# Performance work log

Measured on AMD Instinct MI355X. Metric: run time of the kernel, lower is better.

## Reference

```python
import jax, jax.numpy as jnp
import numpy as np

B, N, D, DG = 32, 2048, 512, 1024


def layernorm(x, g, b, eps=1e-5):
    m = jnp.mean(x, axis=-1, keepdims=True)
    v = jnp.mean((x - m) ** 2, axis=-1, keepdims=True)
    return (x - m) * jax.lax.rsqrt(v + eps) * g + b


def simple_rms_norm(x, eps=1e-6):
    # parameter-free RMSNorm used inside Hgru1d
    return x * jax.lax.rsqrt(jnp.mean(x * x, axis=-1, keepdims=True) + eps)


def linear_recurrence(lam, u, reverse):
    # h_t = lam_t * h_{t-1} + u_t along axis=1, via associative scan
    def comb(c1, c2):
        a1, b1 = c1
        a2, b2 = c2
        return a1 * a2, a2 * b1 + b2
    return jax.lax.associative_scan(comb, (lam, u), axis=1, reverse=reverse)[1]


def hgru1d(x, lower_bound, Wi, bi, Wf, bf, Wg, bg, Wo, bo):
    # HGRN-style gated recurrence, bidirectional (causal=False, shared params)
    i = jax.nn.silu(x @ Wi + bi)                       # candidate input  [b,n,d]
    f = jax.nn.sigmoid(x @ Wf + bf)                    # forget gate      [b,n,d]
    lam = lower_bound + (1.0 - lower_bound) * f        # lower-bounded decay
    u = (1.0 - lam) * i
    h = linear_recurrence(lam, u, False) + linear_recurrence(lam, u, True)
    h = simple_rms_norm(h)
    g = jax.nn.sigmoid(x @ Wg + bg)                    # output gate
    return (h * g) @ Wo + bo


def glu(x, W1, b1, W2, b2, W3, b3):
    return (jax.nn.silu(x @ W1 + b1) * (x @ W2 + b2)) @ W3 + b3


def setup_inputs() -> dict:
    key = jax.random.key(0)
    ks = jax.random.split(key, 16)
    s = 0.02
    return {
        "x": jax.random.normal(ks[0], (B, N, D), dtype=jnp.float32),
        "lower_bound": 0,
        "Wi": jax.random.normal(ks[1], (D, D), jnp.float32) * s,
        "bi": jnp.zeros((D,), jnp.float32),
        "Wf": jax.random.normal(ks[2], (D, D), jnp.float32) * s,
        "bf": jnp.zeros((D,), jnp.float32),
        "Wg": jax.random.normal(ks[3], (D, D), jnp.float32) * s,
        "bg": jnp.zeros((D,), jnp.float32),
        "Wo": jax.random.normal(ks[4], (D, D), jnp.float32) * s,
        "bo": jnp.zeros((D,), jnp.float32),
        "tn_g": jnp.ones((D,), jnp.float32),
        "tn_b": jnp.zeros((D,), jnp.float32),
        "fn_g": jnp.ones((D,), jnp.float32),
        "fn_b": jnp.zeros((D,), jnp.float32),
        "W1": jax.random.normal(ks[5], (D, DG), jnp.float32) * s,
        "b1": jnp.zeros((DG,), jnp.float32),
        "W2": jax.random.normal(ks[6], (D, DG), jnp.float32) * s,
        "b2": jnp.zeros((DG,), jnp.float32),
        "W3": jax.random.normal(ks[7], (DG, D), jnp.float32) * s,
        "b3": jnp.zeros((D,), jnp.float32),
    }


def reference(x, lower_bound, Wi, bi, Wf, bf, Wg, bg, Wo, bo,
              tn_g, tn_b, fn_g, fn_b, W1, b1, W2, b2, W3, b3):
    lb = jnp.float32(lower_bound)
    # post-norm residual block
    x = x + layernorm(hgru1d(x, lb, Wi, bi, Wf, bf, Wg, bg, Wo, bo), tn_g, tn_b)
    x = x + layernorm(glu(x, W1, b1, W2, b2, W3, b3), fn_g, fn_b)
    return x
```

## Files before the change

kernel.cpp:

```cpp
#include <hip/hip_runtime.h>
#include <hip/hip_bf16.h>

#define BB 32
#define NN 2048
#define DD 512
#define DGG 1024
#define CC 32
#define LLEN 64

typedef short bf16x8 __attribute__((ext_vector_type(8)));
typedef float f32x4  __attribute__((ext_vector_type(4)));

__device__ __forceinline__ unsigned short f2bf(float f){
    __hip_bfloat16 h = __float2bfloat16(f);
    return *reinterpret_cast<unsigned short*>(&h);
}
__device__ __forceinline__ float bf2f(unsigned short u){
    unsigned int x = ((unsigned int)u) << 16;
    return __uint_as_float(x);
}
__device__ __forceinline__ float sigm(float x){ return 1.0f/(1.0f + __expf(-x)); }

__device__ __forceinline__ void gl_lds16(const unsigned short* g, unsigned short* l){
    __builtin_amdgcn_global_load_lds(
        (const __attribute__((address_space(1))) unsigned int*)g,
        (__attribute__((address_space(3))) unsigned int*)l, 16, 0, 0);
}

__global__ __launch_bounds__(256)
void wt_prep(const float* __restrict__ in, unsigned short* __restrict__ out,
             int K, int N)
{
    __shared__ float t[32][33];
    const int tid = threadIdx.x;
    const int r = tid >> 3;
    const int c = (tid & 7) << 2;
    const int n0 = blockIdx.x * 32;
    const int k0 = blockIdx.y * 32;
    float4 v = *(const float4*)(in + (size_t)(k0 + r) * N + n0 + c);
    t[r][c] = v.x; t[r][c+1] = v.y; t[r][c+2] = v.z; t[r][c+3] = v.w;
    __syncthreads();
    ushort4 o;
    o.x = f2bf(t[c+0][r]); o.y = f2bf(t[c+1][r]);
    o.z = f2bf(t[c+2][r]); o.w = f2bf(t[c+3][r]);
    *(ushort4*)(out + (size_t)(n0 + r) * K + k0 + c) = o;
}

__global__ __launch_bounds__(256)
void wt_prep_pair(const float* __restrict__ in0, const float* __restrict__ in1,
                  unsigned short* __restrict__ out, int K, int N)
{
    __shared__ float t[32][33];
    const int tid = threadIdx.x;
    const int bx  = blockIdx.x;
    const int k0  = blockIdx.y * 32;
    const int kk  = tid >> 3;
    const int rq  = (tid & 7) << 2;
    const float* src = ((rq >> 4) & 1) ? in1 : in0;
    const int c0 = bx * 16 + (rq & 15);
    float4 v = *(const float4*)(src + (size_t)(k0 + kk) * N + c0);
    t[kk][rq] = v.x; t[kk][rq+1] = v.y; t[kk][rq+2] = v.z; t[kk][rq+3] = v.w;
    __syncthreads();
    const int rr = tid >> 3;
    const int kc = (tid & 7) << 2;
    ushort4 o;
    o.x = f2bf(t[kc+0][rr]); o.y = f2bf(t[kc+1][rr]);
    o.z = f2bf(t[kc+2][rr]); o.w = f2bf(t[kc+3][rr]);
    *(ushort4*)(out + (size_t)(bx * 32 + rr) * K + k0 + kc) = o;
}

__global__ __launch_bounds__(256)
void cast_bf16(const float* __restrict__ in, unsigned short* __restrict__ out)
{
    size_t i = ((size_t)blockIdx.x * 256 + threadIdx.x) * 4;
    float4 v = *(const float4*)(in + i);
    ushort4 o;
    o.x = f2bf(v.x); o.y = f2bf(v.y); o.z = f2bf(v.z); o.w = f2bf(v.w);
    *(ushort4*)(out + i) = o;
}

template<int MODE, int K, int NI>
__global__ __launch_bounds__(512, 2)
void gemm256(const unsigned short* __restrict__ A,
             const unsigned short* __restrict__ Bt,
             const float* __restrict__ bias0,
             const float* __restrict__ bias1,
             unsigned short* __restrict__ out0,
             unsigned short* __restrict__ out1,
             const int* __restrict__ lbp, int Mtiles)
{
    constexpr int NT   = K / 32;
    constexpr int Ntl  = NI / 256;
    constexpr int NOUT = (MODE >= 5) ? NI / 2 : NI;
    constexpr int TILE = 256 * 32;
    __shared__ unsigned short As0[TILE], As1[TILE], As2[TILE], As3[TILE];
    __shared__ unsigned short Bs0[TILE], Bs1[TILE], Bs2[TILE], Bs3[TILE];
#define ASL(i) ((i)==0?As0:(i)==1?As1:(i)==2?As2:As3)
#define BSL(i) ((i)==0?Bs0:(i)==1?Bs1:(i)==2?Bs2:Bs3)

    const int tid  = threadIdx.x;
    const int wave = tid >> 6;
    const int lane = tid & 63;
    const int lm   = lane & 15;
    const int quad = lane >> 4;
    const int wr   = (wave >> 2) * 128;
    const int wc   = (wave & 3) * 64;

    const int nwg = Mtiles * Ntl;
    const int h   = blockIdx.x;
    const int wg  = (h & 7) * (nwg >> 3) + (h >> 3);
    const int bm  = wg / Ntl;
    const int bn  = wg - bm * Ntl;
    const size_t m0 = (size_t)bm * 256;
    const int    n0 = bn * 256;

    const int lrow  = lane >> 2;
    const int oslot = ((lane & 3) ^ ((lane >> 3) & 3)) << 3;
    const unsigned short* gA = A  + (m0 + (size_t)(wave * 16 + lrow)) * K + oslot;
    const unsigned short* gB = Bt + ((size_t)n0 + wave * 16 + lrow) * K + oslot;
    const int lbase = (wave * 16) * 32;
    const int aslot = (quad ^ ((lm >> 1) & 3)) << 3;

#define STAGE(kt, i) do {                                               \
        const unsigned short* ga_ = gA + (kt) * 32;                     \
        const unsigned short* gb_ = gB + (kt) * 32;                     \
        gl_lds16(ga_,                  ASL(i) + lbase);                 \
        gl_lds16(ga_ + (size_t)128*K,  ASL(i) + lbase + 128*32);        \
        gl_lds16(gb_,                  BSL(i) + lbase);                 \
        gl_lds16(gb_ + (size_t)128*K,  BSL(i) + lbase + 128*32);        \
    } while (0)

    f32x4 acc[8][4];
    const f32x4 zero = {0.f, 0.f, 0.f, 0.f};
    #pragma unroll
    for (int i = 0; i < 8; ++i)
        #pragma unroll
        for (int j = 0; j < 4; ++j) acc[i][j] = zero;

    STAGE(0, 0);
    STAGE(1, 1);
    STAGE(2, 2);
    asm volatile("s_waitcnt vmcnt(8)" ::: "memory");
    __builtin_amdgcn_s_barrier();

    #pragma unroll
    for (int t = 0; t < NT; ++t) {
        if (t + 3 < NT) STAGE(t + 3, (t + 3) & 3);

        const unsigned short* Ab = ASL(t & 3);
        const unsigned short* Bb = BSL(t & 3);
        bf16x8 a[8], b[4];
        #pragma unroll
        for (int mi = 0; mi < 8; ++mi)
            a[mi] = *(const bf16x8*)&Ab[(wr + mi * 16 + lm) * 32 + aslot];
        #pragma unroll
        for (int ni = 0; ni < 4; ++ni)
            b[ni] = *(const bf16x8*)&Bb[(wc + ni * 16 + lm) * 32 + aslot];
        #pragma unroll
        for (int mi = 0; mi < 8; ++mi)
            #pragma unroll
            for (int ni = 0; ni < 4; ++ni)
                acc[mi][ni] = __builtin_amdgcn_mfma_f32_16x16x32_bf16(
                    a[mi], b[ni], acc[mi][ni], 0, 0, 0);

        if (t + 1 < NT) {
            if (t + 3 < NT)      asm volatile("s_waitcnt vmcnt(8)" ::: "memory");
            else if (t + 2 < NT) asm volatile("s_waitcnt vmcnt(4)" ::: "memory");
            else                 asm volatile("s_waitcnt vmcnt(0)" ::: "memory");
            __builtin_amdgcn_s_barrier();
        }
    }
#undef STAGE
#undef ASL
#undef BSL

    float lbv = 0.f;
    if constexpr (MODE == 5) lbv = (float)(*lbp);

    if constexpr (MODE == 5 || MODE == 6) {
        const int cbase = (n0 + wc) >> 1;
        #pragma unroll
        for (int nip = 0; nip < 4; nip += 2) {
            const int c = cbase + (nip >> 1) * 16 + lm;
            const float b0 = bias0[c];
            const float b1v = bias1[c];
            #pragma unroll
            for (int mi = 0; mi < 8; ++mi) {
                #pragma unroll
                for (int r = 0; r < 4; ++r) {
                    const size_t row = m0 + wr + mi * 16 + quad * 4 + r;
                    const size_t oidx = row * NOUT + c;
                    float p0 = acc[mi][nip][r]     + b0;
                    float p1 = acc[mi][nip + 1][r] + b1v;
                    if constexpr (MODE == 5) {
                        float si = p0 * sigm(p0);
                        float fv = sigm(p1);
                        float lamv = lbv + (1.f - lbv) * fv;
                        out0[oidx] = f2bf(lamv);
                        out1[oidx] = f2bf((1.f - lamv) * si);
                    } else {
                        out0[oidx] = f2bf(p0 * sigm(p0) * p1);
                    }
                }
            }
        }
    } else {
        #pragma unroll
        for (int ni = 0; ni < 4; ++ni) {
            const int col = n0 + wc + ni * 16 + lm;
            const float bcol = bias0[col];
            #pragma unroll
            for (int mi = 0; mi < 8; ++mi) {
                #pragma unroll
                for (int r = 0; r < 4; ++r) {
                    const size_t row = m0 + wr + mi * 16 + quad * 4 + r;
                    const size_t oidx = row * NOUT + col;
                    float v = acc[mi][ni][r] + bcol;
                    if constexpr (MODE == 0) out0[oidx] = f2bf(v);
                    else                     out0[oidx] = f2bf(sigm(v));
                }
            }
        }
    }
}

__global__ __launch_bounds__(512)
void scan_agg(const unsigned short* __restrict__ lam, const unsigned short* __restrict__ u,
              float* __restrict__ Aarr, float* __restrict__ Vf, float* __restrict__ Vr)
{
    int bc = blockIdx.x;
    int b = bc >> 5, c = bc & 31;
    int d = threadIdx.x;
    size_t base = ((size_t)b * NN + c * LLEN) * DD + d;
    float A = 1.f, vf = 0.f, vr = 0.f;
    for (int t = 0; t < LLEN; ++t) {
        float lv = bf2f(lam[base + (size_t)t * DD]);
        float uv = bf2f(u[base + (size_t)t * DD]);
        vf = lv * vf + uv;
        vr += uv * A;
        A *= lv;
    }
    size_t o = (size_t)bc * DD + d;
    Aarr[o] = A; Vf[o] = vf; Vr[o] = vr;
}

__global__ __launch_bounds__(256)
void scan_comb(const float* __restrict__ Aarr, const float* __restrict__ Vf,
               const float* __restrict__ Vr, float* __restrict__ cf, float* __restrict__ cr)
{
    int g = blockIdx.x * 256 + threadIdx.x;
    int b = g >> 9, d = g & 511;
    float S = 0.f;
    for (int c = 0; c < CC; ++c) {
        size_t o = (size_t)(b * CC + c) * DD + d;
        cf[o] = S;
        S = Vf[o] + Aarr[o] * S;
    }
    S = 0.f;
    for (int c = CC - 1; c >= 0; --c) {
        size_t o = (size_t)(b * CC + c) * DD + d;
        cr[o] = S;
        S = Vr[o] + Aarr[o] * S;
    }
}

__global__ __launch_bounds__(256)
void scan_final(const unsigned short* __restrict__ lam, const unsigned short* __restrict__ u,
                const float* __restrict__ cf, const float* __restrict__ cr,
                float* __restrict__ h)
{
    int bid = blockIdx.x;
    int dh = bid & 1, c = (bid >> 1) & 31, b = bid >> 6;
    int d = dh * 256 + threadIdx.x;
    size_t base = ((size_t)b * NN + c * LLEN) * DD + d;
    size_t co   = (size_t)(b * CC + c) * DD + d;

    float hbuf[LLEN];
    float hf = cf[co];
    #pragma unroll
    for (int t = 0; t < LLEN; ++t) {
        float lv = bf2f(lam[base + (size_t)t * DD]);
        float uv = bf2f(u[base + (size_t)t * DD]);
        hf = lv * hf + uv;
        hbuf[t] = hf;
    }
    float hr = cr[co];
    #pragma unroll
    for (int t = LLEN - 1; t >= 0; --t) {
        float lv = bf2f(lam[base + (size_t)t * DD]);
        float uv = bf2f(u[base + (size_t)t * DD]);
        hr = lv * hr + uv;
        h[base + (size_t)t * DD] = hbuf[t] + hr;
    }
}

__global__ __launch_bounds__(256)
void rms_mul(const float* __restrict__ h, const unsigned short* __restrict__ g,
             unsigned short* __restrict__ hg)
{
    int row = blockIdx.x;
    size_t base = (size_t)row * DD;
    int tid = threadIdx.x, col = tid * 2;
    float2 v = *(const float2*)&h[base + col];
    float ss = v.x * v.x + v.y * v.y;
    #pragma unroll
    for (int off = 32; off > 0; off >>= 1) ss += __shfl_down(ss, off);
    __shared__ float ps[4];
    __shared__ float scale_s;
    if ((tid & 63) == 0) ps[tid >> 6] = ss;
    __syncthreads();
    if (tid == 0) scale_s = rsqrtf((ps[0] + ps[1] + ps[2] + ps[3]) * (1.f / DD) + 1e-6f);
    __syncthreads();
    float sc = scale_s;
    ushort2 gv = *(const ushort2*)&g[base + col];
    ushort2 o;
    o.x = f2bf(v.x * sc * bf2f(gv.x));
    o.y = f2bf(v.y * sc * bf2f(gv.y));
    *(ushort2*)&hg[base + col] = o;
}

__global__ __launch_bounds__(256)
void add_ln(const float* __restrict__ xin, const unsigned short* __restrict__ y,
            const float* __restrict__ gam, const float* __restrict__ bet,
            float* __restrict__ out, unsigned short* __restrict__ outb)
{
    int row = blockIdx.x;
    size_t base = (size_t)row * DD;
    int tid = threadIdx.x, col = tid * 2;
    ushort2 yv = *(const ushort2*)&y[base + col];
    float vx = bf2f(yv.x), vy = bf2f(yv.y);
    float s = vx + vy;
    float ss = vx * vx + vy * vy;
    #pragma unroll
    for (int off = 32; off > 0; off >>= 1) {
        s  += __shfl_down(s, off);
        ss += __shfl_down(ss, off);
    }
    __shared__ float ps[8];
    __shared__ float stats[2];
    if ((tid & 63) == 0) { ps[tid >> 6] = s; ps[4 + (tid >> 6)] = ss; }
    __syncthreads();
    if (tid == 0) {
        float st  = ps[0] + ps[1] + ps[2] + ps[3];
        float sst = ps[4] + ps[5] + ps[6] + ps[7];
        float mean = st * (1.f / DD);
        float var  = sst * (1.f / DD) - mean * mean;
        stats[0] = mean; stats[1] = rsqrtf(var + 1e-5f);
    }
    __syncthreads();
    float mean = stats[0], inv = stats[1];
    float2 xv = *(const float2*)&xin[base + col];
    float2 gv = *(const float2*)&gam[col];
    float2 bv = *(const float2*)&bet[col];
    float2 o;
    o.x = xv.x + (vx - mean) * inv * gv.x + bv.x;
    o.y = xv.y + (vy - mean) * inv * gv.y + bv.y;
    *(float2*)&out[base + col] = o;
    if (outb) {
        ushort2 ob; ob.x = f2bf(o.x); ob.y = f2bf(o.y);
        *(ushort2*)&outb[base + col] = ob;
    }
}

extern "C" void kernel_launch(void* const* d_in, const int* in_sizes, int n_in,
                              void* d_out, int out_size, void* d_ws, size_t ws_size,
                              hipStream_t stream)
{
    const float* x   = (const float*)d_in[0];
    const int*   lb  = (const int*)d_in[1];
    const float* Wi  = (const float*)d_in[2];
    const float* bi  = (const float*)d_in[3];
    const float* Wf  = (const float*)d_in[4];
    const float* bfp = (const float*)d_in[5];
    const float* Wg  = (const float*)d_in[6];
    const float* bg  = (const float*)d_in[7];
    const float* Wo  = (const float*)d_in[8];
    const float* bo  = (const float*)d_in[9];
    const float* tng = (const float*)d_in[10];
    const float* tnb = (const float*)d_in[11];
    const float* fng = (const float*)d_in[12];
    const float* fnb = (const float*)d_in[13];
    const float* W1  = (const float*)d_in[14];
    const float* b1  = (const float*)d_in[15];
    const float* W2  = (const float*)d_in[16];
    const float* b2  = (const float*)d_in[17];
    const float* W3  = (const float*)d_in[18];
    const float* b3  = (const float*)d_in[19];

    unsigned short* wbase = (unsigned short*)d_ws;
    unsigned short* WifT = wbase;
    unsigned short* WgT  = WifT + 524288;
    unsigned short* WoT  = WgT + 262144;
    unsigned short* W12T = WoT + 262144;
    unsigned short* W3T  = W12T + 1048576;
    const size_t WTOT = 524288 + 262144 + 262144 + 1048576 + 524288;

    wt_prep_pair<<<dim3(32, 16), 256, 0, stream>>>(Wi, Wf, WifT, 512, 512);
    wt_prep<<<dim3(16, 16), 256, 0, stream>>>(Wg, WgT, 512, 512);
    wt_prep<<<dim3(16, 16), 256, 0, stream>>>(Wo, WoT, 512, 512);
    wt_prep_pair<<<dim3(64, 16), 256, 0, stream>>>(W1, W2, W12T, 512, 1024);
    wt_prep<<<dim3(16, 32), 256, 0, stream>>>(W3, W3T, 1024, 512);

    const size_t perB = (size_t)4 * NN * DD * 2 + (size_t)5 * CC * DD * 4;
    int Bch = 32;
    while (Bch > 1 && WTOT * 2 + (size_t)Bch * perB > ws_size) Bch >>= 1;
    const int nch = BB / Bch;

    const size_t slabE = (size_t)Bch * NN * DD;

    for (int ch = 0; ch < nch; ++ch) {
        const size_t r0 = (size_t)ch * Bch * NN;
        const int Mc = Bch * NN;
        const int Mt = Mc / 256;
        const float* xc = x + r0 * DD;
        unsigned short* S0 = wbase + WTOT;
        unsigned short* S1 = S0 + slabE;
        unsigned short* S2 = S0 + 2 * slabE;
        unsigned short* S3 = S0 + 3 * slabE;
        float* small = (float*)(S0 + 4 * slabE);
        const size_t agg = (size_t)Bch * CC * DD;
        float* Aarr = small;
        float* VfP  = small + agg;
        float* VrP  = small + 2 * agg;
        float* cfP  = small + 3 * agg;
        float* crP  = small + 4 * agg;
        float* hout = (float*)d_out + r0 * DD;

        cast_bf16<<<Mc / 2, 256, 0, stream>>>(xc, S3);
        gemm256<5, 512, 1024><<<Mt * 4, 512, 0, stream>>>(
            S3, WifT, bi, bfp, S1, S0, lb, Mt);
        gemm256<2, 512, 512><<<Mt * 2, 512, 0, stream>>>(
            S3, WgT, bg, nullptr, S2, nullptr, nullptr, Mt);
        scan_agg<<<Bch * CC, 512, 0, stream>>>(S1, S0, Aarr, VfP, VrP);
        scan_comb<<<(Bch * DD) / 256, 256, 0, stream>>>(Aarr, VfP, VrP, cfP, crP);
        scan_final<<<Bch * CC * 2, 256, 0, stream>>>(S1, S0, cfP, crP, hout);
        rms_mul<<<Mc, 256, 0, stream>>>(hout, S2, S2);
        gemm256<0, 512, 512><<<Mt * 2, 512, 0, stream>>>(
            S2, WoT, bo, nullptr, S0, nullptr, nullptr, Mt);
        add_ln<<<Mc, 256, 0, stream>>>(xc, S0, tng, tnb, hout, S3);
        gemm256<6, 512, 2048><<<Mt * 8, 512, 0, stream>>>(
            S3, W12T, b1, b2, S1, nullptr, nullptr, Mt);
        gemm256<0, 1024, 512><<<Mt * 2, 512, 0, stream>>>(
            S1, W3T, b3, nullptr, S0, nullptr, nullptr, Mt);
        add_ln<<<Mc, 256, 0, stream>>>(hout, S0, fng, fnb, hout, nullptr);
    }
}
```

Before: 1.266 ms.

## Rewrite GEMM main loop as 8-phase ping-pong schedule with 64-wide K tiles

Replaces the 4-stage, 32-wide-K software pipeline in the bf16 MFMA GEMM with a double-buffered 64-wide-K scheme. Each K tile is split into four quadrant phases that interleave LDS reads, async global-to-LDS loads and MFMA bursts, separated by barriers and raised wave priority. The aim is to overlap memory traffic with matrix math more finely and issue fewer, larger K steps. The cost is many more barriers per iteration and a new XOR swizzle for 64-element rows, which could hurt if the sync overhead dominates. LDS use is unchanged at 128 KB.

```diff
diff --git a/kernel.cpp b/kernel.cpp
--- a/kernel.cpp
+++ b/kernel.cpp
@@ -81,22 +81,20 @@
 
 template<int MODE, int K, int NI>
 __global__ __launch_bounds__(512, 2)
-void gemm256(const unsigned short* __restrict__ A,
-             const unsigned short* __restrict__ Bt,
-             const float* __restrict__ bias0,
-             const float* __restrict__ bias1,
-             unsigned short* __restrict__ out0,
-             unsigned short* __restrict__ out1,
-             const int* __restrict__ lbp, int Mtiles)
-{
-    constexpr int NT   = K / 32;
-    constexpr int Ntl  = NI / 256;
-    constexpr int NOUT = (MODE >= 5) ? NI / 2 : NI;
-    constexpr int TILE = 256 * 32;
-    __shared__ unsigned short As0[TILE], As1[TILE], As2[TILE], As3[TILE];
-    __shared__ unsigned short Bs0[TILE], Bs1[TILE], Bs2[TILE], Bs3[TILE];
-#define ASL(i) ((i)==0?As0:(i)==1?As1:(i)==2?As2:As3)
-#define BSL(i) ((i)==0?Bs0:(i)==1?Bs1:(i)==2?Bs2:Bs3)
+void gemm8p(const unsigned short* __restrict__ A,
+            const unsigned short* __restrict__ Bt,
+            const float* __restrict__ bias0,
+            const float* __restrict__ bias1,
+            unsigned short* __restrict__ out0,
+            unsigned short* __restrict__ out1,
+            const int* __restrict__ lbp, int Mtiles)
+{
+    constexpr int NKT   = K / 64;
+    constexpr int ITERS = NKT / 2;
+    constexpr int Ntl   = NI / 256;
+    constexpr int NOUT  = (MODE >= 5) ? NI / 2 : NI;
+    __shared__ unsigned short As0[256*64], As1[256*64];
+    __shared__ unsigned short Bs0[256*64], Bs1[256*64];
 
     const int tid  = threadIdx.x;
     const int wave = tid >> 6;
@@ -107,72 +105,115 @@
     const int wc   = (wave & 3) * 64;
 
     const int nwg = Mtiles * Ntl;
-    const int h   = blockIdx.x;
-    const int wg  = (h & 7) * (nwg >> 3) + (h >> 3);
+    const int hb  = blockIdx.x;
+    const int wg  = (hb & 7) * (nwg >> 3) + (hb >> 3);
     const int bm  = wg / Ntl;
     const int bn  = wg - bm * Ntl;
     const size_t m0 = (size_t)bm * 256;
     const int    n0 = bn * 256;
 
-    const int lrow  = lane >> 2;
-    const int oslot = ((lane & 3) ^ ((lane >> 3) & 3)) << 3;
-    const unsigned short* gA = A  + (m0 + (size_t)(wave * 16 + lrow)) * K + oslot;
-    const unsigned short* gB = Bt + ((size_t)n0 + wave * 16 + lrow) * K + oslot;
-    const int lbase = (wave * 16) * 32;
-    const int aslot = (quad ^ ((lm >> 1) & 3)) << 3;
-
-#define STAGE(kt, i) do {                                               \
-        const unsigned short* ga_ = gA + (kt) * 32;                     \
-        const unsigned short* gb_ = gB + (kt) * 32;                     \
-        gl_lds16(ga_,                  ASL(i) + lbase);                 \
-        gl_lds16(ga_ + (size_t)128*K,  ASL(i) + lbase + 128*32);        \
-        gl_lds16(gb_,                  BSL(i) + lbase);                 \
-        gl_lds16(gb_ + (size_t)128*K,  BSL(i) + lbase + 128*32);        \
+    const int r8 = lane >> 3;
+    const int sl = (lane & 7) ^ r8;
+    const unsigned short* gA = A  + (m0 + wave * 8 + r8) * (size_t)K + sl * 8;
+    const unsigned short* gB = Bt + ((size_t)n0 + wave * 8 + r8) * K + sl * 8;
+    const int ldw = wave * 8 * 64;
+    const int sx  = lm & 7;
+
+#define STG(XS, gX, kt, hh) do {                                              \
+        gl_lds16(gX + (size_t)((hh)*128)      * K + (kt)*64,                  \
+                 XS + ((hh)*128)      * 64 + ldw);                            \
+        gl_lds16(gX + (size_t)((hh)*128 + 64) * K + (kt)*64,                  \
+                 XS + ((hh)*128 + 64) * 64 + ldw);                            \
     } while (0)
 
+#define MFQ(mh, nh, bsel) do {                                                \
+        _Pragma("unroll") for (int ks = 0; ks < 2; ++ks)                      \
+        _Pragma("unroll") for (int mi = 0; mi < 4; ++mi)                      \
+        _Pragma("unroll") for (int ni = 0; ni < 2; ++ni)                      \
+            acc[(mh)*4+mi][(nh)*2+ni] = __builtin_amdgcn_mfma_f32_16x16x32_bf16( \
+                a[mi][ks], bsel[ni][ks], acc[(mh)*4+mi][(nh)*2+ni], 0, 0, 0); \
+    } while (0)
+
+#define RD_A(XS, mh) do {                                                     \
+        _Pragma("unroll") for (int ks = 0; ks < 2; ++ks)                      \
+        _Pragma("unroll") for (int mi = 0; mi < 4; ++mi)                      \
+            a[mi][ks] = *(const bf16x8*)&XS[(wr + ((mh)*4+mi)*16 + lm)*64     \
+                                            + ((ks*4+quad) ^ sx)*8];          \
+    } while (0)
+#define RD_B(XS, nh, breg) do {                                               \
+        _Pragma("unroll") for (int ks = 0; ks < 2; ++ks)                      \
+        _Pragma("unroll") for (int ni = 0; ni < 2; ++ni)                      \
+            breg[ni][ks] = *(const bf16x8*)&XS[(wc + ((nh)*2+ni)*16 + lm)*64  \
+                                               + ((ks*4+quad) ^ sx)*8];       \
+    } while (0)
+
+#define BARRIER()  __builtin_amdgcn_s_barrier()
+#define LGKM0()    asm volatile("s_waitcnt lgkmcnt(0)" ::: "memory")
+#define VMC(n)     asm volatile("s_waitcnt vmcnt(" #n ")" ::: "memory")
+
     f32x4 acc[8][4];
-    const f32x4 zero = {0.f, 0.f, 0.f, 0.f};
     #pragma unroll
     for (int i = 0; i < 8; ++i)
         #pragma unroll
-        for (int j = 0; j < 4; ++j) acc[i][j] = zero;
-
-    STAGE(0, 0);
-    STAGE(1, 1);
-    STAGE(2, 2);
-    asm volatile("s_waitcnt vmcnt(8)" ::: "memory");
-    __builtin_amdgcn_s_barrier();
-
-    #pragma unroll
-    for (int t = 0; t < NT; ++t) {
-        if (t + 3 < NT) STAGE(t + 3, (t + 3) & 3);
-
-        const unsigned short* Ab = ASL(t & 3);
-        const unsigned short* Bb = BSL(t & 3);
-        bf16x8 a[8], b[4];
-        #pragma unroll
-        for (int mi = 0; mi < 8; ++mi)
-            a[mi] = *(const bf16x8*)&Ab[(wr + mi * 16 + lm) * 32 + aslot];
-        #pragma unroll
-        for (int ni = 0; ni < 4; ++ni)
-            b[ni] = *(const bf16x8*)&Bb[(wc + ni * 16 + lm) * 32 + aslot];
-        #pragma unroll
-        for (int mi = 0; mi < 8; ++mi)
-            #pragma unroll
-            for (int ni = 0; ni < 4; ++ni)
-                acc[mi][ni] = __builtin_amdgcn_mfma_f32_16x16x32_bf16(
-                    a[mi], b[ni], acc[mi][ni], 0, 0, 0);
-
-        if (t + 1 < NT) {
-            if (t + 3 < NT)      asm volatile("s_waitcnt vmcnt(8)" ::: "memory");
-            else if (t + 2 < NT) asm volatile("s_waitcnt vmcnt(4)" ::: "memory");
-            else                 asm volatile("s_waitcnt vmcnt(0)" ::: "memory");
-            __builtin_amdgcn_s_barrier();
-        }
-    }
-#undef STAGE
-#undef ASL
-#undef BSL
+        for (int j = 0; j < 4; ++j) acc[i][j] = (f32x4){0.f, 0.f, 0.f, 0.f};
+
+    bf16x8 a[4][2], bA[2][2], bB[2][2];
+
+    STG(Bs0, gB, 0, 0); STG(As0, gA, 0, 0); STG(As0, gA, 0, 1);
+    STG(Bs0, gB, 0, 1); STG(Bs1, gB, 1, 0); STG(As1, gA, 1, 0);
+    VMC(4);
+    BARRIER();
+
+    #pragma unroll
+    for (int j = 0; j < ITERS; ++j) {
+        const bool LAST = (j == ITERS - 1);
+        RD_A(As0, 0); RD_B(Bs0, 0, bA);
+        STG(As1, gA, 2*j + 1, 1);
+        BARRIER(); LGKM0();
+        __builtin_amdgcn_s_setprio(1); MFQ(0, 0, bA); __builtin_amdgcn_s_setprio(0);
+        BARRIER();
+        RD_B(Bs0, 1, bB);
+        STG(Bs1, gB, 2*j + 1, 1);
+        BARRIER(); LGKM0();
+        __builtin_amdgcn_s_setprio(1); MFQ(0, 1, bB); __builtin_amdgcn_s_setprio(0);
+        BARRIER();
+        RD_A(As0, 1);
+        if (2*j + 2 < NKT) STG(Bs0, gB, 2*j + 2, 0);
+        BARRIER(); LGKM0();
+        __builtin_amdgcn_s_setprio(1); MFQ(1, 0, bA); __builtin_amdgcn_s_setprio(0);
+        BARRIER();
+        if (2*j + 2 < NKT) STG(As0, gA, 2*j + 2, 0);
+        BARRIER(); LGKM0();
+        __builtin_amdgcn_s_setprio(1); MFQ(1, 1, bB); __builtin_amdgcn_s_setprio(0);
+        if (LAST) { VMC(0); } else { VMC(4); }
+        BARRIER();
+        RD_A(As1, 0); RD_B(Bs1, 0, bA);
+        if (2*j + 2 < NKT) STG(As0, gA, 2*j + 2, 1);
+        BARRIER(); LGKM0();
+        __builtin_amdgcn_s_setprio(1); MFQ(0, 0, bA); __builtin_amdgcn_s_setprio(0);
+        BARRIER();
+        RD_B(Bs1, 1, bB);
+        if (2*j + 2 < NKT) STG(Bs0, gB, 2*j + 2, 1);
+        BARRIER(); LGKM0();
+        __builtin_amdgcn_s_setprio(1); MFQ(0, 1, bB); __builtin_amdgcn_s_setprio(0);
+        BARRIER();
+        RD_A(As1, 1);
+        if (2*j + 3 < NKT) STG(Bs1, gB, 2*j + 3, 0);
+        BARRIER(); LGKM0();
+        __builtin_amdgcn_s_setprio(1); MFQ(1, 0, bA); __builtin_amdgcn_s_setprio(0);
+        BARRIER();
+        if (2*j + 3 < NKT) STG(As1, gA, 2*j + 3, 0);
+        BARRIER(); LGKM0();
+        __builtin_amdgcn_s_setprio(1); MFQ(1, 1, bB); __builtin_amdgcn_s_setprio(0);
+        if (!LAST) { VMC(4); BARRIER(); }
+    }
+#undef STG
+#undef MFQ
+#undef RD_A
+#undef RD_B
+#undef BARRIER
+#undef LGKM0
+#undef VMC
 
     float lbv = 0.f;
     if constexpr (MODE == 5) lbv = (float)(*lbp);
@@ -427,20 +468,20 @@
         float* hout = (float*)d_out + r0 * DD;
 
         cast_bf16<<<Mc / 2, 256, 0, stream>>>(xc, S3);
-        gemm256<5, 512, 1024><<<Mt * 4, 512, 0, stream>>>(
+        gemm8p<5, 512, 1024><<<Mt * 4, 512, 0, stream>>>(
             S3, WifT, bi, bfp, S1, S0, lb, Mt);
-        gemm256<2, 512, 512><<<Mt * 2, 512, 0, stream>>>(
+        gemm8p<2, 512, 512><<<Mt * 2, 512, 0, stream>>>(
             S3, WgT, bg, nullptr, S2, nullptr, nullptr, Mt);
         scan_agg<<<Bch * CC, 512, 0, stream>>>(S1, S0, Aarr, VfP, VrP);
         scan_comb<<<(Bch * DD) / 256, 256, 0, stream>>>(Aarr, VfP, VrP, cfP, crP);
         scan_final<<<Bch * CC * 2, 256, 0, stream>>>(S1, S0, cfP, crP, hout);
         rms_mul<<<Mc, 256, 0, stream>>>(hout, S2, S2);
-        gemm256<0, 512, 512><<<Mt * 2, 512, 0, stream>>>(
+        gemm8p<0, 512, 512><<<Mt * 2, 512, 0, stream>>>(
             S2, WoT, bo, nullptr, S0, nullptr, nullptr, Mt);
         add_ln<<<Mc, 256, 0, stream>>>(xc, S0, tng, tnb, hout, S3);
-        gemm256<6, 512, 2048><<<Mt * 8, 512, 0, stream>>>(
+        gemm8p<6, 512, 2048><<<Mt * 8, 512, 0, stream>>>(
             S3, W12T, b1, b2, S1, nullptr, nullptr, Mt);
-        gemm256<0, 1024, 512><<<Mt * 2, 512, 0, stream>>>(
+        gemm8p<0, 1024, 512><<<Mt * 2, 512, 0, stream>>>(
             S1, W3T, b3, nullptr, S0, nullptr, nullptr, Mt);
         add_ln<<<Mc, 256, 0, stream>>>(hout, S0, fng, fnb, hout, nullptr);
     }
```

New measurement: 1.115 ms. 11.9% less time.
